# Performance work log

Measured on AMD Instinct MI355X. Metric: run time of the kernel, lower is better.

## Reference

```python
import jax, jax.numpy as jnp
import numpy as np

# pywt.Wavelet('db4') decomposition low-pass; rec_lo = dec_lo[::-1], rec_hi[n] = (-1)^n * dec_lo[n]
DB4_DEC_LO = np.array([-0.010597401784997278, 0.032883011666982945, 0.030841381835986965,
                       -0.18703481171888114, -0.02798376941698385, 0.6308807679295904,
                       0.7148465705525415, 0.23037781330885523], dtype=np.float32)
FILTER_LEN = 8
PAD_L, PAD_R = 3, 4  # TF 'SAME' padding for filter 8, stride 1: total 7, left 3, right 4


def _upsample2(z):
    # zero-insertion upsample: out[:, ::2, :] = z, out[:, 1::2, :] = 0
    B, L, C = z.shape
    return jnp.stack([z, jnp.zeros_like(z)], axis=2).reshape(B, 2 * L, C)


def _same_corr(z, f):
    # per-channel cross-correlation with shared 1D filter f (len 8), TF SAME padding
    C = z.shape[-1]
    zp = jnp.pad(z, ((0, 0), (PAD_L, PAD_R), (0, 0)))
    k = jnp.tile(f[:, None, None], (1, 1, C))  # [W, in/groups=1, out=C]
    return jax.lax.conv_general_dilated(
        zp, k, window_strides=(1,), padding='VALID',
        dimension_numbers=('NWC', 'WIO', 'NWC'), feature_group_count=C)


def setup_inputs() -> dict:
    key = jax.random.key(0)
    inputs = jax.random.normal(key, (16, 16000, 128), dtype=jnp.float32)
    rec_lo = jnp.asarray(DB4_DEC_LO[::-1].copy())
    rec_hi = jnp.asarray((((-1.0) ** np.arange(FILTER_LEN)).astype(np.float32)) * DB4_DEC_LO)
    return {"inputs": inputs, "rec_lo": rec_lo, "rec_hi": rec_hi}


def reference(inputs, rec_lo, rec_hi):
    C = inputs.shape[-1] // 2
    approx_up = _upsample2(inputs[:, :, :C])   # [B, 2L, C]
    detail_up = _upsample2(inputs[:, :, C:])   # [B, 2L, C]
    return _same_corr(approx_up, rec_lo) + _same_corr(detail_up, rec_hi)
```

## Files before the change

### kernel.cpp

```cpp
#include <hip/hip_runtime.h>


#define NB 16
#define NL 16000
#define MBLK 1000

__global__ __launch_bounds__(256) void idwt_db4_kernel(
    const float* __restrict__ in,
    const float* __restrict__ rec_lo,
    const float* __restrict__ rec_hi,
    float* __restrict__ out)
{
    const int tid = threadIdx.x;
    const int c  = (tid & 15) * 4;
    const int ml = tid >> 4;
    const int blk = blockIdx.x;
    const int b = blk / MBLK;
    const int m = (blk - b * MBLK) * 16 + ml;

    float lo[8], hi[8];
#pragma unroll
    for (int i = 0; i < 8; ++i) { lo[i] = rec_lo[i]; hi[i] = rec_hi[i]; }

    const long inBase = (long)b * NL * 128 + c;

    float4 a[4], d[4];
#pragma unroll
    for (int k = 0; k < 4; ++k) {
        const int l = m - 1 + k;
        if (l >= 0 && l < NL) {
            const float4* p = (const float4*)(in + inBase + (long)l * 128);
            a[k] = p[0];
            d[k] = p[16];
        } else {
            a[k] = make_float4(0.f, 0.f, 0.f, 0.f);
            d[k] = make_float4(0.f, 0.f, 0.f, 0.f);
        }
    }

    float4 ev = make_float4(0.f, 0.f, 0.f, 0.f);
    float4 od = make_float4(0.f, 0.f, 0.f, 0.f);
#pragma unroll
    for (int k = 0; k < 4; ++k) {
        const float leA = lo[2*k + 1], leD = hi[2*k + 1];
        const float loA = lo[2*k],     loD = hi[2*k];
        ev.x = fmaf(a[k].x, leA, fmaf(d[k].x, leD, ev.x));
        ev.y = fmaf(a[k].y, leA, fmaf(d[k].y, leD, ev.y));
        ev.z = fmaf(a[k].z, leA, fmaf(d[k].z, leD, ev.z));
        ev.w = fmaf(a[k].w, leA, fmaf(d[k].w, leD, ev.w));
        od.x = fmaf(a[k].x, loA, fmaf(d[k].x, loD, od.x));
        od.y = fmaf(a[k].y, loA, fmaf(d[k].y, loD, od.y));
        od.z = fmaf(a[k].z, loA, fmaf(d[k].z, loD, od.z));
        od.w = fmaf(a[k].w, loA, fmaf(d[k].w, loD, od.w));
    }

    const long outBase = ((long)b * (2 * NL) + 2 * m) * 64 + c;
    *(float4*)(out + outBase)      = ev;
    *(float4*)(out + outBase + 64) = od;
}

extern "C" void kernel_launch(void* const* d_in, const int* in_sizes, int n_in,
                              void* d_out, int out_size, void* d_ws, size_t ws_size,
                              hipStream_t stream)
{
    const float* in     = (const float*)d_in[0];
    const float* rec_lo = (const float*)d_in[1];
    const float* rec_hi = (const float*)d_in[2];
    float* out = (float*)d_out;

    dim3 grid(NB * MBLK);
    dim3 block(256);
    idwt_db4_kernel<<<grid, block, 0, stream>>>(in, rec_lo, rec_hi, out);
}
```

Before: 48.07 us.

## Compute four output positions per thread with register reuse and nontemporal stores

Each thread now handles four consecutive input positions and loads a sliding window of seven rows instead of four rows per output, so overlapping input rows are reused from registers rather than reloaded. The grid shrinks accordingly. Output writes use nontemporal stores to avoid polluting cache with streaming data. The cost is more registers per thread and fewer blocks in flight.

Result: slower. 85.12 us (+77.1%).

```diff
diff --git a/kernel.cpp b/kernel.cpp
--- a/kernel.cpp
+++ b/kernel.cpp
@@ -3,7 +3,11 @@
 
 #define NB 16
 #define NL 16000
-#define MBLK 1000
+#define MPT 4
+#define MBLOCK 64
+#define NMB (NL / MBLOCK)
+
+typedef float fx4 __attribute__((ext_vector_type(4)));
 
 __global__ __launch_bounds__(256) void idwt_db4_kernel(
     const float* __restrict__ in,
@@ -13,10 +17,10 @@
 {
     const int tid = threadIdx.x;
     const int c  = (tid & 15) * 4;
-    const int ml = tid >> 4;
+    const int g  = tid >> 4;
     const int blk = blockIdx.x;
-    const int b = blk / MBLK;
-    const int m = (blk - b * MBLK) * 16 + ml;
+    const int b = blk / NMB;
+    const int m0 = (blk - b * NMB) * MBLOCK + g * MPT;
 
     float lo[8], hi[8];
 #pragma unroll
@@ -24,39 +28,39 @@
 
     const long inBase = (long)b * NL * 128 + c;
 
-    float4 a[4], d[4];
+    fx4 A[MPT + 3], D[MPT + 3];
 #pragma unroll
-    for (int k = 0; k < 4; ++k) {
-        const int l = m - 1 + k;
+    for (int r = 0; r < MPT + 3; ++r) {
+        const int l = m0 - 1 + r;
         if (l >= 0 && l < NL) {
-            const float4* p = (const float4*)(in + inBase + (long)l * 128);
-            a[k] = p[0];
-            d[k] = p[16];
+            const fx4* p = (const fx4*)(in + inBase + (long)l * 128);
+            A[r] = p[0];
+            D[r] = p[16];
         } else {
-            a[k] = make_float4(0.f, 0.f, 0.f, 0.f);
-            d[k] = make_float4(0.f, 0.f, 0.f, 0.f);
+            A[r] = (fx4)(0.f);
+            D[r] = (fx4)(0.f);
         }
     }
 
-    float4 ev = make_float4(0.f, 0.f, 0.f, 0.f);
-    float4 od = make_float4(0.f, 0.f, 0.f, 0.f);
+    const long outBase0 = ((long)b * (2 * NL) + 2 * m0) * 64 + c;
+
 #pragma unroll
-    for (int k = 0; k < 4; ++k) {
-        const float leA = lo[2*k + 1], leD = hi[2*k + 1];
-        const float loA = lo[2*k],     loD = hi[2*k];
-        ev.x = fmaf(a[k].x, leA, fmaf(d[k].x, leD, ev.x));
-        ev.y = fmaf(a[k].y, leA, fmaf(d[k].y, leD, ev.y));
-        ev.z = fmaf(a[k].z, leA, fmaf(d[k].z, leD, ev.z));
-        ev.w = fmaf(a[k].w, leA, fmaf(d[k].w, leD, ev.w));
-        od.x = fmaf(a[k].x, loA, fmaf(d[k].x, loD, od.x));
-        od.y = fmaf(a[k].y, loA, fmaf(d[k].y, loD, od.y));
-        od.z = fmaf(a[k].z, loA, fmaf(d[k].z, loD, od.z));
-        od.w = fmaf(a[k].w, loA, fmaf(d[k].w, loD, od.w));
+    for (int j = 0; j < MPT; ++j) {
+        fx4 ev = (fx4)(0.f);
+        fx4 od = (fx4)(0.f);
+#pragma unroll
+        for (int k = 0; k < 4; ++k) {
+            const fx4 a = A[j + k], d = D[j + k];
+            const float leA = lo[2*k + 1], leD = hi[2*k + 1];
+            const float loA = lo[2*k],     loD = hi[2*k];
+            ev = a * leA + (d * leD + ev);
+            od = a * loA + (d * loD + od);
+        }
+        float* pe = out + outBase0 + (long)j * 128;
+        float* po = pe + 64;
+        __builtin_nontemporal_store(ev, (fx4*)pe);
+        __builtin_nontemporal_store(od, (fx4*)po);
     }
-
-    const long outBase = ((long)b * (2 * NL) + 2 * m) * 64 + c;
-    *(float4*)(out + outBase)      = ev;
-    *(float4*)(out + outBase + 64) = od;
 }
 
 extern "C" void kernel_launch(void* const* d_in, const int* in_sizes, int n_in,
@@ -68,7 +72,7 @@
     const float* rec_hi = (const float*)d_in[2];
     float* out = (float*)d_out;
 
-    dim3 grid(NB * MBLK);
+    dim3 grid(NB * NMB);
     dim3 block(256);
     idwt_db4_kernel<<<grid, block, 0, stream>>>(in, rec_lo, rec_hi, out);
 }
```
